# Performance work log

Measured on AMD Instinct MI355X. Metric: run time of the kernel, lower is better.

Reference implementation:

```python
import jax, jax.numpy as jnp
import numpy as np

N = 100000   # nodes
E = 1600000  # edges (avg degree 16)
IN = 64
HID = 16     # hardcoded in ChebNet.conv1
OUT = 40
K = 3


def setup_inputs() -> dict:
    key = jax.random.key(0)
    k0, k1, k2, k3 = jax.random.split(key, 4)
    x = jax.random.normal(k0, (N, IN), jnp.float32)
    edge_index = jax.random.randint(k1, (2, E), 0, N, jnp.int32)
    # Glorot-style init for the K per-order linear maps of each ChebConv
    s1 = float(np.sqrt(2.0 / (IN + HID)))
    W1 = jax.random.normal(k2, (K, IN, HID), jnp.float32) * s1
    b1 = jnp.zeros((HID,), jnp.float32)
    s2 = float(np.sqrt(2.0 / (HID + OUT)))
    W2 = jax.random.normal(k3, (K, HID, OUT), jnp.float32) * s2
    b2 = jnp.zeros((OUT,), jnp.float32)
    return {"x": x, "edge_index": edge_index, "W1": W1, "b1": b1, "W2": W2, "b2": b2}


def cheb_conv(x, edge_index, W, b):
    """PyG ChebConv with normalization='sym', lambda_max=2.
    Scaled Laplacian: L_hat = 2L/lambda_max - I = -D^{-1/2} A D^{-1/2} (diag 0).
    out = sum_k T_k(L_hat) x @ W[k] + b, T0=x, T1=L_hat x, Tk=2 L_hat T_{k-1}-T_{k-2}.
    """
    row, col = edge_index[0], edge_index[1]
    ones = jnp.ones((edge_index.shape[1],), x.dtype)
    deg = jax.ops.segment_sum(ones, row, num_segments=N)
    dis = jnp.where(deg > 0, jax.lax.rsqrt(jnp.maximum(deg, 1.0)), 0.0)
    norm = -(dis[row] * dis[col])  # [E]

    def Lhat(z):  # sparse scatter-gather: gather src rows, scale, scatter-add to dst
        return jax.ops.segment_sum(norm[:, None] * z[row], col, num_segments=N)

    Tx0 = x
    out = Tx0 @ W[0]
    Tx1 = Lhat(x)
    if W.shape[0] > 1:
        out = out + Tx1 @ W[1]
    for k in range(2, W.shape[0]):
        Tx2 = 2.0 * Lhat(Tx1) - Tx0
        out = out + Tx2 @ W[k]
        Tx0, Tx1 = Tx1, Tx2
    return out + b


def reference(x, edge_index, W1, b1, W2, b2):
    h = jax.nn.relu(cheb_conv(x, edge_index, W1, b1))
    h = cheb_conv(h, edge_index, W2, b2)
    return jax.nn.log_softmax(h, axis=1)
```

## Files before the change

### kernel.cpp

```cpp
#include <hip/hip_runtime.h>
#include <hip/hip_bf16.h>


typedef unsigned short u16;

constexpr int N_    = 100000;
constexpr int E_    = 1600000;
constexpr int IN_   = 64;
constexpr int HID_  = 16;
constexpr int OUT_  = 40;
constexpr int CAP_  = 48;
constexpr int S_    = 64;
constexpr int EPS_  = E_ / S_;
constexpr int P8_   = 8;
constexpr int NPP8_ = N_ / P8_;
constexpr int P4_   = 4;
constexpr int NPP4_ = N_ / P4_;
constexpr int NPAD_ = 100352;

__device__ __forceinline__ float bf2f(u16 u) {
    return __uint_as_float((unsigned)u << 16);
}
__device__ __forceinline__ u16 f2bf(float x) {
    unsigned u = __float_as_uint(x);
    return (u16)((u + 0x7FFFu + ((u >> 16) & 1u)) >> 16);
}

__global__ void deg_part(const int* __restrict__ row, u16* __restrict__ partial) {
    __shared__ int lds[NPP8_];
    int p = blockIdx.x >> 6, s = blockIdx.x & 63;
    for (int i = threadIdx.x; i < NPP8_; i += 256) lds[i] = 0;
    __syncthreads();
    int lo = p * NPP8_, e0 = s * EPS_;
    for (int i = threadIdx.x; i < EPS_; i += 256) {
        int r = row[e0 + i];
        unsigned d = (unsigned)(r - lo);
        if (d < (unsigned)NPP8_) atomicAdd(&lds[d], 1);
    }
    __syncthreads();
    u16* dst = partial + (size_t)blockIdx.x * NPP8_;
    for (int i = threadIdx.x; i < NPP8_; i += 256) dst[i] = (u16)lds[i];
}

__global__ void __launch_bounds__(1024)
hist_in(const int* __restrict__ col, u16* __restrict__ partial) {
    __shared__ int lds[NPP4_];
    int p = blockIdx.x >> 6, s = blockIdx.x & 63;
    for (int i = threadIdx.x; i < NPP4_; i += 1024) lds[i] = 0;
    __syncthreads();
    int lo = p * NPP4_, e0 = s * EPS_;
    for (int i = threadIdx.x; i < EPS_; i += 1024) {
        int c = col[e0 + i];
        unsigned d = (unsigned)(c - lo);
        if (d < (unsigned)NPP4_) atomicAdd(&lds[d], 1);
    }
    __syncthreads();
    u16* dst = partial + (size_t)blockIdx.x * NPP4_;
    for (int i = threadIdx.x; i < NPP4_; i += 1024) dst[i] = (u16)lds[i];
}

__global__ void __launch_bounds__(1024)
reduce_all(const u16* __restrict__ partial_row, const u16* __restrict__ partial_in,
           float* __restrict__ dis, u16* __restrict__ pre, int* __restrict__ indeg) {
    int n = blockIdx.x * 1024 + threadIdx.x;
    if (n >= N_) return;
    {
        int p = n / NPP8_, i = n - p * NPP8_;
        const u16* base = partial_row + (size_t)(p * S_) * NPP8_ + i;
        int d = 0;
#pragma unroll 8
        for (int s = 0; s < S_; ++s) d += base[(size_t)s * NPP8_];
        dis[n] = (d > 0) ? rsqrtf((float)d) : 0.0f;
    }
    {
        int p = n / NPP4_, i = n - p * NPP4_;
        const u16* base = partial_in + (size_t)(p * S_) * NPP4_ + i;
        int run = 0;
#pragma unroll 8
        for (int s = 0; s < S_; ++s) {
            pre[(size_t)s * NPAD_ + n] = (u16)run;
            run += base[(size_t)s * NPP4_];
        }
        indeg[n] = run;
    }
}

__global__ void __launch_bounds__(1024)
place_proj(const int* __restrict__ row, const int* __restrict__ col,
           const float* __restrict__ x, const float* __restrict__ W,
           const float* __restrict__ dis, const u16* __restrict__ pre,
           int* __restrict__ bucket,
           float* __restrict__ P0f, float* __restrict__ P2f,
           u16* __restrict__ A1, u16* __restrict__ A2) {
    __shared__ int pos[NPP4_];
    __shared__ float w[3 * IN_ * HID_];
    if (blockIdx.x < 256) {
        int p = blockIdx.x >> 6, s = blockIdx.x & 63;
        int lo = p * NPP4_, e0 = s * EPS_;
        const u16* psrc = pre + (size_t)s * NPAD_ + lo;
        for (int i = threadIdx.x; i < NPP4_; i += 1024) pos[i] = psrc[i];
        __syncthreads();
        for (int i = threadIdx.x; i < EPS_; i += 1024) {
            int c = col[e0 + i];
            unsigned d = (unsigned)(c - lo);
            if (d < (unsigned)NPP4_) {
                int r = row[e0 + i];
                int q = atomicAdd(&pos[d], 1);
                if (q < CAP_) bucket[(size_t)c * CAP_ + q] = r;
            }
        }
    } else {
        for (int i = threadIdx.x; i < 3 * IN_ * HID_; i += 1024) w[i] = W[i];
        __syncthreads();
        int t = (blockIdx.x - 256) * 1024 + threadIdx.x;
        if (t >= N_ * HID_) return;
        int n = t >> 4, j = t & 15;
        const float* xr = x + (size_t)n * IN_;
        float a0 = 0.f, a1 = 0.f, a2 = 0.f;
#pragma unroll
        for (int i = 0; i < IN_; ++i) {
            float xv = xr[i];
            a0 += xv * w[i * 16 + j];
            a1 += xv * w[1024 + i * 16 + j];
            a2 += xv * w[2048 + i * 16 + j];
        }
        float dn = dis[n];
        P0f[t] = a0;
        P2f[t] = a2;
        A1[t] = f2bf(dn * a1);
        A2[t] = f2bf(dn * a2);
    }
}

__global__ void g32b(const u16* __restrict__ A1, const u16* __restrict__ A2,
                     const int* __restrict__ indeg, const int* __restrict__ bucket,
                     const float* __restrict__ dis,
                     float* __restrict__ LP1f, u16* __restrict__ B2) {
    int wib = threadIdx.x >> 6, lane = threadIdx.x & 63;
    int n0 = (blockIdx.x * 4 + wib) * 4;
    int eg = lane >> 3, sub = lane & 7;
    const u16* Z = (sub < 4) ? A1 : A2;
    int fq = sub & 3;
    int m[4];
#pragma unroll
    for (int k = 0; k < 4; ++k) m[k] = min(indeg[n0 + k], CAP_);
    float ax[4] = {0,0,0,0}, ay[4] = {0,0,0,0}, az[4] = {0,0,0,0}, aw[4] = {0,0,0,0};
#pragma unroll
    for (int k = 0; k < 4; ++k) {
        int n = n0 + k;
        for (int base = 0; base < m[k]; base += 8) {
            int e = base + eg;
            if (e < m[k]) {
                int r = bucket[n * CAP_ + e];
                ushort4 zv = *(const ushort4*)&Z[(size_t)r * 16 + fq * 4];
                ax[k] += bf2f(zv.x); ay[k] += bf2f(zv.y);
                az[k] += bf2f(zv.z); aw[k] += bf2f(zv.w);
            }
        }
    }
#pragma unroll
    for (int off = 8; off < 64; off <<= 1) {
#pragma unroll
        for (int k = 0; k < 4; ++k) {
            ax[k] += __shfl_xor(ax[k], off, 64); ay[k] += __shfl_xor(ay[k], off, 64);
            az[k] += __shfl_xor(az[k], off, 64); aw[k] += __shfl_xor(aw[k], off, 64);
        }
    }
    if (lane < 8) {
#pragma unroll
        for (int k = 0; k < 4; ++k) {
            int n = n0 + k;
            float dn = dis[n];
            if (lane < 4) {
                float4 v = {-dn * ax[k], -dn * ay[k], -dn * az[k], -dn * aw[k]};
                *(float4*)&LP1f[(size_t)n * 16 + fq * 4] = v;
            } else {
                float s = -(dn * dn);
                ushort4 v = {f2bf(s * ax[k]), f2bf(s * ay[k]),
                             f2bf(s * az[k]), f2bf(s * aw[k])};
                *(ushort4*)&B2[(size_t)n * 16 + fq * 4] = v;
            }
        }
    }
}

__device__ __forceinline__ void g16core4(const u16* __restrict__ Z,
                                         const int* __restrict__ indeg,
                                         const int* __restrict__ bucket,
                                         int n0, int lane, float4 acc[4]) {
    int eg = lane >> 2, fq = lane & 3;
    int m[4];
#pragma unroll
    for (int k = 0; k < 4; ++k) m[k] = min(indeg[n0 + k], CAP_);
    float ax[4] = {0,0,0,0}, ay[4] = {0,0,0,0}, az[4] = {0,0,0,0}, aw[4] = {0,0,0,0};
#pragma unroll
    for (int k = 0; k < 4; ++k) {
        int n = n0 + k;
        for (int base = 0; base < m[k]; base += 16) {
            int e = base + eg;
            if (e < m[k]) {
                int r = bucket[n * CAP_ + e];
                ushort4 zv = *(const ushort4*)&Z[(size_t)r * 16 + fq * 4];
                ax[k] += bf2f(zv.x); ay[k] += bf2f(zv.y);
                az[k] += bf2f(zv.z); aw[k] += bf2f(zv.w);
            }
        }
    }
#pragma unroll
    for (int off = 4; off < 64; off <<= 1) {
#pragma unroll
        for (int k = 0; k < 4; ++k) {
            ax[k] += __shfl_xor(ax[k], off, 64); ay[k] += __shfl_xor(ay[k], off, 64);
            az[k] += __shfl_xor(az[k], off, 64); aw[k] += __shfl_xor(aw[k], off, 64);
        }
    }
#pragma unroll
    for (int k = 0; k < 4; ++k) {
        float4 r4 = {ax[k], ay[k], az[k], aw[k]};
        acc[k] = r4;
    }
}

__global__ void g16_combine(const u16* __restrict__ B2, const int* __restrict__ indeg,
                            const int* __restrict__ bucket, const float* __restrict__ dis,
                            const float* __restrict__ LP1f, const float* __restrict__ P2f,
                            const float* __restrict__ b1,
                            float* p0h , u16* __restrict__ Hs) {
    int wib = threadIdx.x >> 6, lane = threadIdx.x & 63;
    int n0 = (blockIdx.x * 4 + wib) * 4;
    float4 acc[4];
    g16core4(B2, indeg, bucket, n0, lane, acc);
    if (lane < 4) {
#pragma unroll
        for (int k = 0; k < 4; ++k) {
            int n = n0 + k;
            float dn = dis[n];
            float4 p0 = *(const float4*)&p0h[(size_t)n * 16 + lane * 4];
            float4 lp = *(const float4*)&LP1f[(size_t)n * 16 + lane * 4];
            float4 p2 = *(const float4*)&P2f[(size_t)n * 16 + lane * 4];
            float4 bb = *(const float4*)&b1[lane * 4];
            float4 hv;
            hv.x = fmaxf(p0.x + lp.x - 2.f * dn * acc[k].x - p2.x + bb.x, 0.f);
            hv.y = fmaxf(p0.y + lp.y - 2.f * dn * acc[k].y - p2.y + bb.y, 0.f);
            hv.z = fmaxf(p0.z + lp.z - 2.f * dn * acc[k].z - p2.z + bb.z, 0.f);
            hv.w = fmaxf(p0.w + lp.w - 2.f * dn * acc[k].w - p2.w + bb.w, 0.f);
            *(float4*)&p0h[(size_t)n * 16 + lane * 4] = hv;
            ushort4 hs = {f2bf(dn * hv.x), f2bf(dn * hv.y),
                          f2bf(dn * hv.z), f2bf(dn * hv.w)};
            *(ushort4*)&Hs[(size_t)n * 16 + lane * 4] = hs;
        }
    }
}

__global__ void g16_t1(const u16* __restrict__ Hs, const int* __restrict__ indeg,
                       const int* __restrict__ bucket, const float* __restrict__ dis,
                       float* __restrict__ T1f, u16* __restrict__ Ts) {
    int wib = threadIdx.x >> 6, lane = threadIdx.x & 63;
    int n0 = (blockIdx.x * 4 + wib) * 4;
    float4 acc[4];
    g16core4(Hs, indeg, bucket, n0, lane, acc);
    if (lane < 4) {
#pragma unroll
        for (int k = 0; k < 4; ++k) {
            int n = n0 + k;
            float dn = dis[n];
            float4 t1 = {-dn * acc[k].x, -dn * acc[k].y, -dn * acc[k].z, -dn * acc[k].w};
            *(float4*)&T1f[(size_t)n * 16 + lane * 4] = t1;
            ushort4 ts = {f2bf(dn * t1.x), f2bf(dn * t1.y),
                          f2bf(dn * t1.z), f2bf(dn * t1.w)};
            *(ushort4*)&Ts[(size_t)n * 16 + lane * 4] = ts;
        }
    }
}

__global__ void g16_mm2_lsm(const u16* __restrict__ Ts, const int* __restrict__ indeg,
                            const int* __restrict__ bucket, const float* __restrict__ dis,
                            const float* __restrict__ Hf, const float* __restrict__ T1f,
                            const float* __restrict__ W2, const float* __restrict__ b2,
                            float* __restrict__ out) {
    __shared__ float w[3 * HID_ * OUT_];
    __shared__ float t2s[4][4][16];
    for (int i = threadIdx.x; i < 3 * HID_ * OUT_; i += blockDim.x) w[i] = W2[i];
    int wib = threadIdx.x >> 6, lane = threadIdx.x & 63;
    int n0 = (blockIdx.x * 4 + wib) * 4;
    float4 acc[4];
    g16core4(Ts, indeg, bucket, n0, lane, acc);
    if (lane < 4) {
#pragma unroll
        for (int k = 0; k < 4; ++k) {
            int n = n0 + k;
            float dn = dis[n];
            float4 h4 = *(const float4*)&Hf[(size_t)n * 16 + lane * 4];
            float4 t2;
            t2.x = -2.f * dn * acc[k].x - h4.x;
            t2.y = -2.f * dn * acc[k].y - h4.y;
            t2.z = -2.f * dn * acc[k].z - h4.z;
            t2.w = -2.f * dn * acc[k].w - h4.w;
            *(float4*)&t2s[wib][k][lane * 4] = t2;
        }
    }
    __syncthreads();
#pragma unroll
    for (int k = 0; k < 4; ++k) {
        int n = n0 + k;
        float a2 = -3.0e38f;
        if (lane < OUT_) {
            a2 = b2[lane];
            const float* hr  = Hf + (size_t)n * 16;
            const float* t1r = T1f + (size_t)n * 16;
#pragma unroll
            for (int j = 0; j < HID_; ++j) {
                a2 += hr[j] * w[j * OUT_ + lane]
                    + t1r[j] * w[640 + j * OUT_ + lane]
                    + t2s[wib][k][j] * w[1280 + j * OUT_ + lane];
            }
        }
        float mx = a2;
#pragma unroll
        for (int off = 32; off > 0; off >>= 1) mx = fmaxf(mx, __shfl_xor(mx, off, 64));
        float ev = (lane < OUT_) ? __expf(a2 - mx) : 0.0f;
        float s = ev;
#pragma unroll
        for (int off = 32; off > 0; off >>= 1) s += __shfl_xor(s, off, 64);
        float ls = logf(s);
        if (lane < OUT_) out[(size_t)n * OUT_ + lane] = a2 - mx - ls;
    }
}


extern "C" void kernel_launch(void* const* d_in, const int* in_sizes, int n_in,
                              void* d_out, int out_size, void* d_ws, size_t ws_size,
                              hipStream_t stream) {
    const float* x  = (const float*)d_in[0];
    const int*   ei = (const int*)d_in[1];
    const float* W1 = (const float*)d_in[2];
    const float* b1 = (const float*)d_in[3];
    const float* W2 = (const float*)d_in[4];
    const float* b2 = (const float*)d_in[5];
    float* out = (float*)d_out;

    const int* row = ei;
    const int* col = ei + E_;

    char* wp = (char*)d_ws;
    float* dis    = (float*)wp;  wp += 401408;
    int*   indeg  = (int*)wp;    wp += 401408;
    int*   bucket = (int*)wp;    wp += (size_t)N_ * CAP_ * 4;
    u16*   pre    = (u16*)wp;    wp += (size_t)S_ * NPAD_ * 2;
    char*  region = wp;
    u16* partial_row = (u16*)region;
    u16* partial_in  = (u16*)(region + 12800000);
    wp = region;
    u16*   A1   = (u16*)wp;   wp += 3211264;
    u16*   A2   = (u16*)wp;   wp += 3211264;
    u16*   B2   = (u16*)wp;   wp += 3211264;
    float* P0f  = (float*)wp; wp += 6422528;
    float* P2f  = (float*)wp; wp += 6422528;
    float* LP1f = (float*)wp; wp += 6422528;

    float* Hf  = P0f;
    u16*   Hs  = A1;
    float* T1f = LP1f;
    u16*   Ts  = A2;

    deg_part<<<P8_ * S_, 256, 0, stream>>>(row, partial_row);
    hist_in<<<P4_ * S_, 1024, 0, stream>>>(col, partial_in);
    reduce_all<<<NPAD_ / 1024, 1024, 0, stream>>>(partial_row, partial_in,
                                                  dis, pre, indeg);
    place_proj<<<256 + 1563, 1024, 0, stream>>>(row, col, x, W1, dis, pre,
                                                bucket, P0f, P2f, A1, A2);

    g32b<<<N_ / 16, 256, 0, stream>>>(A1, A2, indeg, bucket, dis, LP1f, B2);
    g16_combine<<<N_ / 16, 256, 0, stream>>>(B2, indeg, bucket, dis, LP1f, P2f, b1,
                                             P0f , Hs);
    g16_t1<<<N_ / 16, 256, 0, stream>>>(Hs, indeg, bucket, dis, T1f, Ts);
    g16_mm2_lsm<<<N_ / 16, 256, 0, stream>>>(Ts, indeg, bucket, dis, Hf, T1f,
                                             W2, b2, out);
}
```

Before: 380.2 us.

## Split final gather from dense layer; compute output row per thread

The fused gather + 48x40 matmul + log_softmax kernel is split in two. One kernel computes T2 and writes it to a reused fp32 buffer. A new kernel assigns one node per thread, keeps the 40 outputs in registers, reads W2 through uniform loads, and writes rows as float4. This removes the idle lanes and the per-wave LDS weight staging of the old lane-per-output scheme, at the cost of an extra global round trip for T2, one more launch, and high register pressure.

```diff
diff --git a/kernel.cpp b/kernel.cpp
--- a/kernel.cpp
+++ b/kernel.cpp
@@ -273,14 +273,9 @@
     }
 }
 
-__global__ void g16_mm2_lsm(const u16* __restrict__ Ts, const int* __restrict__ indeg,
-                            const int* __restrict__ bucket, const float* __restrict__ dis,
-                            const float* __restrict__ Hf, const float* __restrict__ T1f,
-                            const float* __restrict__ W2, const float* __restrict__ b2,
-                            float* __restrict__ out) {
-    __shared__ float w[3 * HID_ * OUT_];
-    __shared__ float t2s[4][4][16];
-    for (int i = threadIdx.x; i < 3 * HID_ * OUT_; i += blockDim.x) w[i] = W2[i];
+__global__ void g16_t2(const u16* __restrict__ Ts, const int* __restrict__ indeg,
+                       const int* __restrict__ bucket, const float* __restrict__ dis,
+                       const float* __restrict__ Hf, float* __restrict__ T2f) {
     int wib = threadIdx.x >> 6, lane = threadIdx.x & 63;
     int n0 = (blockIdx.x * 4 + wib) * 4;
     float4 acc[4];
@@ -296,34 +291,52 @@
             t2.y = -2.f * dn * acc[k].y - h4.y;
             t2.z = -2.f * dn * acc[k].z - h4.z;
             t2.w = -2.f * dn * acc[k].w - h4.w;
-            *(float4*)&t2s[wib][k][lane * 4] = t2;
-        }
-    }
-    __syncthreads();
-#pragma unroll
-    for (int k = 0; k < 4; ++k) {
-        int n = n0 + k;
-        float a2 = -3.0e38f;
-        if (lane < OUT_) {
-            a2 = b2[lane];
-            const float* hr  = Hf + (size_t)n * 16;
-            const float* t1r = T1f + (size_t)n * 16;
-#pragma unroll
-            for (int j = 0; j < HID_; ++j) {
-                a2 += hr[j] * w[j * OUT_ + lane]
-                    + t1r[j] * w[640 + j * OUT_ + lane]
-                    + t2s[wib][k][j] * w[1280 + j * OUT_ + lane];
-            }
-        }
-        float mx = a2;
-#pragma unroll
-        for (int off = 32; off > 0; off >>= 1) mx = fmaxf(mx, __shfl_xor(mx, off, 64));
-        float ev = (lane < OUT_) ? __expf(a2 - mx) : 0.0f;
-        float s = ev;
-#pragma unroll
-        for (int off = 32; off > 0; off >>= 1) s += __shfl_xor(s, off, 64);
-        float ls = logf(s);
-        if (lane < OUT_) out[(size_t)n * OUT_ + lane] = a2 - mx - ls;
+            *(float4*)&T2f[(size_t)n * 16 + lane * 4] = t2;
+        }
+    }
+}
+
+__global__ void __launch_bounds__(256)
+mm2_lsm(const float* __restrict__ Hf, const float* __restrict__ T1f,
+        const float* __restrict__ T2f, const float* __restrict__ W2,
+        const float* __restrict__ b2, float* __restrict__ out) {
+    int n = blockIdx.x * 256 + threadIdx.x;
+    if (n >= N_) return;
+    float act[48];
+#pragma unroll
+    for (int q = 0; q < 4; ++q)
+        *(float4*)&act[q * 4] = *(const float4*)&Hf[(size_t)n * 16 + q * 4];
+#pragma unroll
+    for (int q = 0; q < 4; ++q)
+        *(float4*)&act[16 + q * 4] = *(const float4*)&T1f[(size_t)n * 16 + q * 4];
+#pragma unroll
+    for (int q = 0; q < 4; ++q)
+        *(float4*)&act[32 + q * 4] = *(const float4*)&T2f[(size_t)n * 16 + q * 4];
+    float acc[OUT_];
+#pragma unroll
+    for (int o = 0; o < OUT_; ++o) acc[o] = b2[o];
+#pragma unroll
+    for (int j = 0; j < HID_; ++j) {
+        float a0 = act[j], a1 = act[16 + j], a2 = act[32 + j];
+#pragma unroll
+        for (int o = 0; o < OUT_; ++o) {
+            acc[o] += a0 * W2[j * OUT_ + o]
+                    + a1 * W2[640 + j * OUT_ + o]
+                    + a2 * W2[1280 + j * OUT_ + o];
+        }
+    }
+    float mx = acc[0];
+#pragma unroll
+    for (int o = 1; o < OUT_; ++o) mx = fmaxf(mx, acc[o]);
+    float s = 0.f;
+#pragma unroll
+    for (int o = 0; o < OUT_; ++o) s += __expf(acc[o] - mx);
+    float ls = mx + logf(s);
+#pragma unroll
+    for (int q = 0; q < 10; ++q) {
+        float4 v = {acc[q * 4] - ls, acc[q * 4 + 1] - ls,
+                    acc[q * 4 + 2] - ls, acc[q * 4 + 3] - ls};
+        *(float4*)&out[(size_t)n * OUT_ + q * 4] = v;
     }
 }
 
@@ -362,6 +375,7 @@
     u16*   Hs  = A1;
     float* T1f = LP1f;
     u16*   Ts  = A2;
+    float* T2f = P2f;
 
     deg_part<<<P8_ * S_, 256, 0, stream>>>(row, partial_row);
     hist_in<<<P4_ * S_, 1024, 0, stream>>>(col, partial_in);
@@ -374,6 +388,6 @@
     g16_combine<<<N_ / 16, 256, 0, stream>>>(B2, indeg, bucket, dis, LP1f, P2f, b1,
                                              P0f , Hs);
     g16_t1<<<N_ / 16, 256, 0, stream>>>(Hs, indeg, bucket, dis, T1f, Ts);
-    g16_mm2_lsm<<<N_ / 16, 256, 0, stream>>>(Ts, indeg, bucket, dis, Hf, T1f,
-                                             W2, b2, out);
-}
+    g16_t2<<<N_ / 16, 256, 0, stream>>>(Ts, indeg, bucket, dis, Hf, T2f);
+    mm2_lsm<<<(N_ + 255) / 256, 256, 0, stream>>>(Hf, T1f, T2f, W2, b2, out);
+}
```

Result: faster. 353.7 us (-7.0%).
